# Optimization experiments

Hardware: AMD Instinct MI355X
Metric: run time of the kernel (lower is better)

The kernel has to match this reference:

```python
import jax, jax.numpy as jnp
import numpy as np
from math import sqrt

DIM = 64
N_HEADS = 12
B, T = 4, 2048


def setup_inputs() -> dict:
    key = jax.random.key(0)
    ks = jax.random.split(key, 5)
    scale = 1.0 / sqrt(DIM)
    x = jax.random.normal(ks[0], (B, T, DIM), dtype=jnp.float32)
    # torch Linear(dim, h*dim) weight is (h*dim, dim); store transposed (dim, h*dim)
    Wq = jax.random.uniform(ks[1], (DIM, N_HEADS * DIM), dtype=jnp.float32, minval=-scale, maxval=scale)
    Wk = jax.random.uniform(ks[2], (DIM, N_HEADS * DIM), dtype=jnp.float32, minval=-scale, maxval=scale)
    Wv = jax.random.uniform(ks[3], (DIM, N_HEADS * DIM), dtype=jnp.float32, minval=-scale, maxval=scale)
    # finalDense: Linear(h*dim, dim) -> stored (h*dim, dim)
    Wo = jax.random.uniform(ks[4], (N_HEADS * DIM, DIM), dtype=jnp.float32,
                            minval=-1.0 / sqrt(N_HEADS * DIM), maxval=1.0 / sqrt(N_HEADS * DIM))
    return {"x": x, "Wq": Wq, "Wk": Wk, "Wv": Wv, "Wo": Wo}


def reference(x, Wq, Wk, Wv, Wo):
    b, t, k = x.shape
    h = Wq.shape[1] // k
    # NOTE: the original module does .view(b,t,h,k).view(b*h,t,k), a flat
    # row-major memory reinterpretation (NOT a head transpose). jnp.reshape
    # is the same flat reshape, so this is faithful.
    Q = (x @ Wq).reshape(b * h, t, k)
    K = (x @ Wk).reshape(b * h, t, k)
    V = (x @ Wv).reshape(b * h, t, k)
    # W[b,i,j] = sum_k K[b,i,k] * Q[b,j,k], scaled; softmax over j (last dim)
    W = jnp.einsum('bik,bjk->bij', K, Q) / sqrt(k)
    W = jax.nn.softmax(W, axis=2)
    Z = jnp.einsum('bij,bjk->bik', W, V)  # (b*h, t, k)
    Z = Z.reshape(b, t, h * k)  # flat reinterpretation, matches torch views
    return Z @ Wo
```

## Files before the change

kernel.cpp:

```cpp
#include <hip/hip_runtime.h>
#include <hip/hip_bf16.h>


#define DIM 64
#define NH 12
#define HD 768
#define BT 8192
#define TSEQ 2048
#define NSLICE 48
#define SLICE (TSEQ*DIM)

#define LDQ 72
#define LDP 72

typedef unsigned short ushort;
typedef __attribute__((ext_vector_type(8))) short bf16x8;
typedef __attribute__((ext_vector_type(4))) float f32x4;

__device__ __forceinline__ float b2f(ushort u) {
    union { unsigned int i; float f; } v; v.i = ((unsigned int)u) << 16; return v.f;
}
__device__ __forceinline__ ushort f2b(float f) {
    union { float f; unsigned int i; } v; v.f = f;
    unsigned int x = v.i;
    return (ushort)((x + 0x7fffu + ((x >> 16) & 1u)) >> 16);
}

__global__ __launch_bounds__(256) void prep_x(
    const float* __restrict__ x, ushort* __restrict__ xb)
{
    int idx = (blockIdx.x * 256 + threadIdx.x) * 8;
    float4 a = *(const float4*)&x[idx];
    float4 b = *(const float4*)&x[idx + 4];
    ushort tmp[8] __attribute__((aligned(16)));
    tmp[0]=f2b(a.x); tmp[1]=f2b(a.y); tmp[2]=f2b(a.z); tmp[3]=f2b(a.w);
    tmp[4]=f2b(b.x); tmp[5]=f2b(b.y); tmp[6]=f2b(b.z); tmp[7]=f2b(b.w);
    *(float4*)&xb[idx] = *(const float4*)tmp;
}

__global__ __launch_bounds__(256) void prep_w(
    const float* __restrict__ Wq, const float* __restrict__ Wk,
    const float* __restrict__ Wv, const float* __restrict__ Wo,
    ushort* __restrict__ Wt, ushort* __restrict__ Wot)
{
    __shared__ float tile[64][65];
    int bx = blockIdx.x, z = blockIdx.y;
    const float* __restrict__ IN = (z == 0) ? Wq : (z == 1) ? Wk : (z == 2) ? Wv : Wo;
    int inStride  = (z < 3) ? HD : DIM;
    int outStride = (z < 3) ? DIM : HD;
    int rbase = (z < 3) ? 0 : bx * 64;
    int cbase = (z < 3) ? bx * 64 : 0;
    ushort* __restrict__ OUT = (z < 3) ? (Wt + (size_t)z * HD * DIM) : Wot;
    int t = threadIdx.x;
    int r = t >> 2, c0 = (t & 3) * 16;
    #pragma unroll
    for (int cc = 0; cc < 16; cc += 4) {
        float4 a = *(const float4*)&IN[(size_t)(rbase + r) * inStride + cbase + c0 + cc];
        tile[r][c0 + cc] = a.x; tile[r][c0 + cc + 1] = a.y;
        tile[r][c0 + cc + 2] = a.z; tile[r][c0 + cc + 3] = a.w;
    }
    __syncthreads();
    int cl = t >> 2, r0 = (t & 3) * 16;
    ushort tmp[16] __attribute__((aligned(16)));
    #pragma unroll
    for (int rr = 0; rr < 16; ++rr) tmp[rr] = f2b(tile[r0 + rr][cl]);
    *(float4*)&OUT[(size_t)(cbase + cl) * outStride + rbase + r0] = *(const float4*)tmp;
    *(float4*)&OUT[(size_t)(cbase + cl) * outStride + rbase + r0 + 8] = *(const float4*)&tmp[8];
}

__global__ __launch_bounds__(256) void qkv_kernel(
    const ushort* __restrict__ xb, const ushort* __restrict__ Wt,
    ushort* __restrict__ Q, ushort* __restrict__ K, ushort* __restrict__ V)
{
    int rowbase = blockIdx.x * 64;
    int ct = blockIdx.y;
    int which = ct / 12;
    int col0 = (ct % 12) * 64;
    const ushort* __restrict__ Wz = Wt + (size_t)which * HD * DIM;
    ushort* __restrict__ Y = (which == 0) ? Q : (which == 1) ? K : V;
    int t = threadIdx.x, w = t >> 6, lane = t & 63;
    int ln = lane & 15, q = lane >> 4;
    int m0 = rowbase + w * 16;

    bf16x8 af0 = *(const bf16x8*)&xb[(size_t)(m0 + ln) * DIM + q * 8];
    bf16x8 af1 = *(const bf16x8*)&xb[(size_t)(m0 + ln) * DIM + 32 + q * 8];
    #pragma unroll
    for (int nt = 0; nt < 4; ++nt) {
        int n = col0 + nt * 16 + ln;
        bf16x8 bf0 = *(const bf16x8*)&Wz[(size_t)n * DIM + q * 8];
        bf16x8 bf1 = *(const bf16x8*)&Wz[(size_t)n * DIM + 32 + q * 8];
        f32x4 acc = (f32x4){0.f, 0.f, 0.f, 0.f};
        acc = __builtin_amdgcn_mfma_f32_16x16x32_bf16(af0, bf0, acc, 0, 0, 0);
        acc = __builtin_amdgcn_mfma_f32_16x16x32_bf16(af1, bf1, acc, 0, 0, 0);
        #pragma unroll
        for (int r = 0; r < 4; ++r)
            Y[(size_t)(m0 + q * 4 + r) * HD + col0 + nt * 16 + ln] = f2b(acc[r]);
    }
}

__global__ __launch_bounds__(256) void vtrans_kernel(
    const ushort* __restrict__ V, ushort* __restrict__ Vt)
{
    __shared__ ushort tile[64 * LDQ];
    int tt = blockIdx.x, s = blockIdx.y;
    const ushort* __restrict__ Vp = V + (size_t)s * SLICE;
    ushort* __restrict__ Vo = Vt + (size_t)s * SLICE;
    int t = threadIdx.x;
    int r = t >> 3, c = (t & 7) * 8;
    *(float4*)&tile[r * LDQ + c] =
        *(const float4*)&Vp[(size_t)(tt * 64 + r) * DIM + c];
    *(float4*)&tile[(r + 32) * LDQ + c] =
        *(const float4*)&Vp[(size_t)(tt * 64 + r + 32) * DIM + c];
    __syncthreads();
    ushort tmp[8] __attribute__((aligned(16)));
    #pragma unroll
    for (int cc = 0; cc < 8; ++cc) tmp[cc] = tile[(c + cc) * LDQ + r];
    *(float4*)&Vo[(size_t)r * TSEQ + tt * 64 + c] = *(const float4*)tmp;
    #pragma unroll
    for (int cc = 0; cc < 8; ++cc) tmp[cc] = tile[(c + cc) * LDQ + r + 32];
    *(float4*)&Vo[(size_t)(r + 32) * TSEQ + tt * 64 + c] = *(const float4*)tmp;
}

__global__ __launch_bounds__(256) void attn_kernel(
    const ushort* __restrict__ Qs, const ushort* __restrict__ Ks,
    const ushort* __restrict__ Vts, ushort* __restrict__ Zs)
{
    const float SCALE2 = 0.18033688011112042f;
    __shared__ ushort Qt[64 * LDQ];
    __shared__ ushort Vtile[64 * LDQ];
    __shared__ ushort Pw[128 * LDP];
    int itile = blockIdx.x, s = blockIdx.y;
    const ushort* __restrict__ Qp = Qs + (size_t)s * SLICE;
    const ushort* __restrict__ Kp = Ks + (size_t)s * SLICE;
    const ushort* __restrict__ Vp = Vts + (size_t)s * SLICE;
    ushort* __restrict__ Zp = Zs + (size_t)s * SLICE;
    int t = threadIdx.x, w = t >> 6, lane = t & 63;
    int ln = lane & 15, q = lane >> 4;

    bf16x8 kf[2][2];
    #pragma unroll
    for (int ih = 0; ih < 2; ++ih) {
        int i0 = itile * 128 + w * 32 + ih * 16 + ln;
        kf[ih][0] = *(const bf16x8*)&Kp[(size_t)i0 * DIM + q * 8];
        kf[ih][1] = *(const bf16x8*)&Kp[(size_t)i0 * DIM + 32 + q * 8];
    }

    f32x4 Of[2][4];
    #pragma unroll
    for (int ih = 0; ih < 2; ++ih)
        #pragma unroll
        for (int dt = 0; dt < 4; ++dt) Of[ih][dt] = (f32x4){0.f, 0.f, 0.f, 0.f};
    float lsum[2] = {0.f, 0.f};
    ushort* Pme = &Pw[w * 32 * LDP];

    int sr = t >> 3, sc = (t & 7) * 8;
    for (int jt = 0; jt < TSEQ; jt += 64) {
        __syncthreads();
        *(float4*)&Qt[sr * LDQ + sc] =
            *(const float4*)&Qp[(size_t)(jt + sr) * DIM + sc];
        *(float4*)&Qt[(sr + 32) * LDQ + sc] =
            *(const float4*)&Qp[(size_t)(jt + sr + 32) * DIM + sc];
        *(float4*)&Vtile[sr * LDQ + sc] =
            *(const float4*)&Vp[(size_t)sr * TSEQ + jt + sc];
        *(float4*)&Vtile[(sr + 32) * LDQ + sc] =
            *(const float4*)&Vp[(size_t)(sr + 32) * TSEQ + jt + sc];
        __syncthreads();

        f32x4 Sf[2][4];
        #pragma unroll
        for (int mt = 0; mt < 4; ++mt) {
            bf16x8 a0 = *(const bf16x8*)&Qt[(mt * 16 + ln) * LDQ + q * 8];
            bf16x8 a1 = *(const bf16x8*)&Qt[(mt * 16 + ln) * LDQ + 32 + q * 8];
            #pragma unroll
            for (int ih = 0; ih < 2; ++ih) {
                f32x4 acc = (f32x4){0.f, 0.f, 0.f, 0.f};
                acc = __builtin_amdgcn_mfma_f32_16x16x32_bf16(a0, kf[ih][0], acc, 0, 0, 0);
                acc = __builtin_amdgcn_mfma_f32_16x16x32_bf16(a1, kf[ih][1], acc, 0, 0, 0);
                Sf[ih][mt] = acc;
            }
        }
        #pragma unroll
        for (int ih = 0; ih < 2; ++ih) {
            #pragma unroll
            for (int mt = 0; mt < 4; ++mt) {
                float p0 = __builtin_amdgcn_exp2f(Sf[ih][mt][0] * SCALE2);
                float p1 = __builtin_amdgcn_exp2f(Sf[ih][mt][1] * SCALE2);
                float p2 = __builtin_amdgcn_exp2f(Sf[ih][mt][2] * SCALE2);
                float p3 = __builtin_amdgcn_exp2f(Sf[ih][mt][3] * SCALE2);
                lsum[ih] += (p0 + p1) + (p2 + p3);
                ushort4 pk;
                pk.x = f2b(p0); pk.y = f2b(p1); pk.z = f2b(p2); pk.w = f2b(p3);
                *(ushort4*)&Pme[(ih * 16 + ln) * LDP + mt * 16 + q * 4] = pk;
            }
        }
        bf16x8 pa[2][2];
        #pragma unroll
        for (int ih = 0; ih < 2; ++ih) {
            pa[ih][0] = *(const bf16x8*)&Pme[(ih * 16 + ln) * LDP + q * 8];
            pa[ih][1] = *(const bf16x8*)&Pme[(ih * 16 + ln) * LDP + 32 + q * 8];
        }
        #pragma unroll
        for (int dt = 0; dt < 4; ++dt) {
            bf16x8 vb0 = *(const bf16x8*)&Vtile[(dt * 16 + ln) * LDQ + q * 8];
            bf16x8 vb1 = *(const bf16x8*)&Vtile[(dt * 16 + ln) * LDQ + 32 + q * 8];
            #pragma unroll
            for (int ih = 0; ih < 2; ++ih) {
                Of[ih][dt] = __builtin_amdgcn_mfma_f32_16x16x32_bf16(pa[ih][0], vb0, Of[ih][dt], 0, 0, 0);
                Of[ih][dt] = __builtin_amdgcn_mfma_f32_16x16x32_bf16(pa[ih][1], vb1, Of[ih][dt], 0, 0, 0);
            }
        }
    }
    float linv_r[2][4];
    #pragma unroll
    for (int ih = 0; ih < 2; ++ih) {
        float l = lsum[ih];
        l += __shfl_xor(l, 16);
        l += __shfl_xor(l, 32);
        float linv = 1.f / l;
        #pragma unroll
        for (int r = 0; r < 4; ++r) linv_r[ih][r] = __shfl(linv, q * 4 + r);
    }
    #pragma unroll
    for (int ih = 0; ih < 2; ++ih)
        #pragma unroll
        for (int dt = 0; dt < 4; ++dt)
            #pragma unroll
            for (int r = 0; r < 4; ++r)
                Pme[(ih * 16 + q * 4 + r) * LDP + dt * 16 + ln] =
                    f2b(Of[ih][dt][r] * linv_r[ih][r]);
    __syncthreads();
    int zr = t >> 1, zc = (t & 1) * 32;
    size_t zoff = (size_t)(itile * 128 + zr) * DIM + zc;
    #pragma unroll
    for (int c4 = 0; c4 < 4; ++c4)
        *(float4*)&Zp[zoff + c4 * 8] = *(const float4*)&Pw[zr * LDP + zc + c4 * 8];
}

__global__ __launch_bounds__(64) void out_kernel(
    const ushort* __restrict__ Z, const ushort* __restrict__ Wot,
    float* __restrict__ out)
{
    int m0 = blockIdx.x * 16;
    int lane = threadIdx.x;
    int ln = lane & 15, q = lane >> 4;
    f32x4 acc[4];
    #pragma unroll
    for (int nt = 0; nt < 4; ++nt) acc[nt] = (f32x4){0.f, 0.f, 0.f, 0.f};
    for (int kc = 0; kc < 24; ++kc) {
        bf16x8 af = *(const bf16x8*)&Z[(size_t)(m0 + ln) * HD + kc * 32 + q * 8];
        #pragma unroll
        for (int nt = 0; nt < 4; ++nt) {
            bf16x8 bf = *(const bf16x8*)&Wot[(size_t)(nt * 16 + ln) * HD + kc * 32 + q * 8];
            acc[nt] = __builtin_amdgcn_mfma_f32_16x16x32_bf16(af, bf, acc[nt], 0, 0, 0);
        }
    }
    #pragma unroll
    for (int nt = 0; nt < 4; ++nt)
        #pragma unroll
        for (int r = 0; r < 4; ++r)
            out[(size_t)(m0 + q * 4 + r) * DIM + nt * 16 + ln] = acc[nt][r];
}

extern "C" void kernel_launch(void* const* d_in, const int* in_sizes, int n_in,
                              void* d_out, int out_size, void* d_ws, size_t ws_size,
                              hipStream_t stream)
{
    const float* x  = (const float*)d_in[0];
    const float* Wq = (const float*)d_in[1];
    const float* Wk = (const float*)d_in[2];
    const float* Wv = (const float*)d_in[3];
    const float* Wo = (const float*)d_in[4];
    float* out = (float*)d_out;

    const size_t n = (size_t)BT * HD;
    ushort* Q   = (ushort*)d_ws;
    ushort* K   = Q + n;
    ushort* V   = K + n;
    ushort* Vt  = V + n;
    ushort* xb  = Vt;
    ushort* Wt  = Vt + (size_t)BT * DIM;
    ushort* Wot = Vt + n;
    ushort* Z   = V;

    prep_x<<<256, 256, 0, stream>>>(x, xb);
    prep_w<<<dim3(12, 4), 256, 0, stream>>>(Wq, Wk, Wv, Wo, Wt, Wot);
    qkv_kernel<<<dim3(128, 36), 256, 0, stream>>>(xb, Wt, Q, K, V);
    vtrans_kernel<<<dim3(32, 48), 256, 0, stream>>>(V, Vt);
    attn_kernel<<<dim3(16, 48), 256, 0, stream>>>(Q, K, Vt, Z);
    out_kernel<<<512, 64, 0, stream>>>(Z, Wot, out);
}
```

Baseline: 208.3 us.

## Restructure attention to single-wave blocks reading Q/V directly, fuse prep kernels

Attention becomes 64-thread blocks, each owning 32 K rows. Q and Vt fragments are loaded straight from global memory into registers, which removes the shared-memory staging and both barriers per tile. The block index is remapped so that 8 slices interleave, likely for L2 locality. Other changes: the x and weight prep kernels merge into one launch, the V transpose uses an XOR-swizzled shared tile with vector stores, and out_kernel doubles rows per block to reuse the Wo fragments. The softmax row sum now adds the truncated bf16 values actually used in P·V. The risk is that each wave re-reads Q and V from L2 with no sharing across waves.

Result: slower. 310.7 us (+49.2%).

```diff
diff --git a/kernel.cpp b/kernel.cpp
--- a/kernel.cpp
+++ b/kernel.cpp
@@ -10,8 +10,8 @@
 #define NSLICE 48
 #define SLICE (TSEQ*DIM)
 
-#define LDQ 72
 #define LDP 72
+#define LDT 72
 
 typedef unsigned short ushort;
 typedef __attribute__((ext_vector_type(8))) short bf16x8;
@@ -26,32 +26,32 @@
     return (ushort)((x + 0x7fffu + ((x >> 16) & 1u)) >> 16);
 }
 
-__global__ __launch_bounds__(256) void prep_x(
-    const float* __restrict__ x, ushort* __restrict__ xb)
-{
-    int idx = (blockIdx.x * 256 + threadIdx.x) * 8;
-    float4 a = *(const float4*)&x[idx];
-    float4 b = *(const float4*)&x[idx + 4];
-    ushort tmp[8] __attribute__((aligned(16)));
-    tmp[0]=f2b(a.x); tmp[1]=f2b(a.y); tmp[2]=f2b(a.z); tmp[3]=f2b(a.w);
-    tmp[4]=f2b(b.x); tmp[5]=f2b(b.y); tmp[6]=f2b(b.z); tmp[7]=f2b(b.w);
-    *(float4*)&xb[idx] = *(const float4*)tmp;
-}
-
-__global__ __launch_bounds__(256) void prep_w(
+__global__ __launch_bounds__(256) void prep_kernel(
+    const float* __restrict__ x,
     const float* __restrict__ Wq, const float* __restrict__ Wk,
     const float* __restrict__ Wv, const float* __restrict__ Wo,
-    ushort* __restrict__ Wt, ushort* __restrict__ Wot)
+    ushort* __restrict__ xb, ushort* __restrict__ Wt, ushort* __restrict__ Wot)
 {
     __shared__ float tile[64][65];
-    int bx = blockIdx.x, z = blockIdx.y;
+    int bx = blockIdx.x;
+    int t = threadIdx.x;
+    if (bx >= 48) {
+        int idx = ((bx - 48) * 256 + t) * 8;
+        float4 a = *(const float4*)&x[idx];
+        float4 b = *(const float4*)&x[idx + 4];
+        ushort tmp[8] __attribute__((aligned(16)));
+        tmp[0]=f2b(a.x); tmp[1]=f2b(a.y); tmp[2]=f2b(a.z); tmp[3]=f2b(a.w);
+        tmp[4]=f2b(b.x); tmp[5]=f2b(b.y); tmp[6]=f2b(b.z); tmp[7]=f2b(b.w);
+        *(float4*)&xb[idx] = *(const float4*)tmp;
+        return;
+    }
+    int z = bx / 12, bt = bx % 12;
     const float* __restrict__ IN = (z == 0) ? Wq : (z == 1) ? Wk : (z == 2) ? Wv : Wo;
     int inStride  = (z < 3) ? HD : DIM;
     int outStride = (z < 3) ? DIM : HD;
-    int rbase = (z < 3) ? 0 : bx * 64;
-    int cbase = (z < 3) ? bx * 64 : 0;
+    int rbase = (z < 3) ? 0 : bt * 64;
+    int cbase = (z < 3) ? bt * 64 : 0;
     ushort* __restrict__ OUT = (z < 3) ? (Wt + (size_t)z * HD * DIM) : Wot;
-    int t = threadIdx.x;
     int r = t >> 2, c0 = (t & 3) * 16;
     #pragma unroll
     for (int cc = 0; cc < 16; cc += 4) {
@@ -101,97 +101,105 @@
 __global__ __launch_bounds__(256) void vtrans_kernel(
     const ushort* __restrict__ V, ushort* __restrict__ Vt)
 {
-    __shared__ ushort tile[64 * LDQ];
+    __shared__ ushort tileT[64 * LDT];
     int tt = blockIdx.x, s = blockIdx.y;
     const ushort* __restrict__ Vp = V + (size_t)s * SLICE;
     ushort* __restrict__ Vo = Vt + (size_t)s * SLICE;
     int t = threadIdx.x;
     int r = t >> 3, c = (t & 7) * 8;
-    *(float4*)&tile[r * LDQ + c] =
-        *(const float4*)&Vp[(size_t)(tt * 64 + r) * DIM + c];
-    *(float4*)&tile[(r + 32) * LDQ + c] =
-        *(const float4*)&Vp[(size_t)(tt * 64 + r + 32) * DIM + c];
+    ushort va[8] __attribute__((aligned(16)));
+    ushort vb[8] __attribute__((aligned(16)));
+    *(float4*)va = *(const float4*)&Vp[(size_t)(tt * 64 + r) * DIM + c];
+    *(float4*)vb = *(const float4*)&Vp[(size_t)(tt * 64 + r + 32) * DIM + c];
+    int g0 = ((r >> 3) ^ (c >> 3)) * 8 + (r & 7);
+    int g1 = (((r + 32) >> 3) ^ (c >> 3)) * 8 + (r & 7);
+    #pragma unroll
+    for (int k = 0; k < 8; ++k) {
+        tileT[(c + k) * LDT + g0] = va[k];
+        tileT[(c + k) * LDT + g1] = vb[k];
+    }
     __syncthreads();
-    ushort tmp[8] __attribute__((aligned(16)));
-    #pragma unroll
-    for (int cc = 0; cc < 8; ++cc) tmp[cc] = tile[(c + cc) * LDQ + r];
-    *(float4*)&Vo[(size_t)r * TSEQ + tt * 64 + c] = *(const float4*)tmp;
-    #pragma unroll
-    for (int cc = 0; cc < 8; ++cc) tmp[cc] = tile[(c + cc) * LDQ + r + 32];
-    *(float4*)&Vo[(size_t)(r + 32) * TSEQ + tt * 64 + c] = *(const float4*)tmp;
-}
-
-__global__ __launch_bounds__(256) void attn_kernel(
+    #pragma unroll
+    for (int j = 0; j < 2; ++j) {
+        int flat = t + 256 * j;
+        int d = flat >> 3, tg = flat & 7;
+        int sg = tg ^ ((d >> 3) & 7);
+        float4 vv = *(const float4*)&tileT[d * LDT + sg * 8];
+        *(float4*)&Vo[(size_t)d * TSEQ + tt * 64 + tg * 8] = vv;
+    }
+}
+
+__global__ __launch_bounds__(64) void attn_kernel(
     const ushort* __restrict__ Qs, const ushort* __restrict__ Ks,
     const ushort* __restrict__ Vts, ushort* __restrict__ Zs)
 {
     const float SCALE2 = 0.18033688011112042f;
-    __shared__ ushort Qt[64 * LDQ];
-    __shared__ ushort Vtile[64 * LDQ];
-    __shared__ ushort Pw[128 * LDP];
-    int itile = blockIdx.x, s = blockIdx.y;
+    __shared__ ushort Pme[32 * LDP];
+    int bid = blockIdx.x;
+    int s = (bid >> 9) * 8 + (bid & 7);
+    int itile = (bid >> 3) & 63;
     const ushort* __restrict__ Qp = Qs + (size_t)s * SLICE;
     const ushort* __restrict__ Kp = Ks + (size_t)s * SLICE;
     const ushort* __restrict__ Vp = Vts + (size_t)s * SLICE;
     ushort* __restrict__ Zp = Zs + (size_t)s * SLICE;
-    int t = threadIdx.x, w = t >> 6, lane = t & 63;
+    int lane = threadIdx.x;
     int ln = lane & 15, q = lane >> 4;
 
     bf16x8 kf[2][2];
     #pragma unroll
     for (int ih = 0; ih < 2; ++ih) {
-        int i0 = itile * 128 + w * 32 + ih * 16 + ln;
+        int i0 = itile * 32 + ih * 16 + ln;
         kf[ih][0] = *(const bf16x8*)&Kp[(size_t)i0 * DIM + q * 8];
         kf[ih][1] = *(const bf16x8*)&Kp[(size_t)i0 * DIM + 32 + q * 8];
     }
-
     f32x4 Of[2][4];
     #pragma unroll
     for (int ih = 0; ih < 2; ++ih)
         #pragma unroll
         for (int dt = 0; dt < 4; ++dt) Of[ih][dt] = (f32x4){0.f, 0.f, 0.f, 0.f};
     float lsum[2] = {0.f, 0.f};
-    ushort* Pme = &Pw[w * 32 * LDP];
-
-    int sr = t >> 3, sc = (t & 7) * 8;
+
     for (int jt = 0; jt < TSEQ; jt += 64) {
-        __syncthreads();
-        *(float4*)&Qt[sr * LDQ + sc] =
-            *(const float4*)&Qp[(size_t)(jt + sr) * DIM + sc];
-        *(float4*)&Qt[(sr + 32) * LDQ + sc] =
-            *(const float4*)&Qp[(size_t)(jt + sr + 32) * DIM + sc];
-        *(float4*)&Vtile[sr * LDQ + sc] =
-            *(const float4*)&Vp[(size_t)sr * TSEQ + jt + sc];
-        *(float4*)&Vtile[(sr + 32) * LDQ + sc] =
-            *(const float4*)&Vp[(size_t)(sr + 32) * TSEQ + jt + sc];
-        __syncthreads();
-
-        f32x4 Sf[2][4];
+        bf16x8 aq[4][2];
         #pragma unroll
         for (int mt = 0; mt < 4; ++mt) {
-            bf16x8 a0 = *(const bf16x8*)&Qt[(mt * 16 + ln) * LDQ + q * 8];
-            bf16x8 a1 = *(const bf16x8*)&Qt[(mt * 16 + ln) * LDQ + 32 + q * 8];
-            #pragma unroll
-            for (int ih = 0; ih < 2; ++ih) {
+            aq[mt][0] = *(const bf16x8*)&Qp[(size_t)(jt + mt * 16 + ln) * DIM + q * 8];
+            aq[mt][1] = *(const bf16x8*)&Qp[(size_t)(jt + mt * 16 + ln) * DIM + 32 + q * 8];
+        }
+        bf16x8 vb[4][2];
+        #pragma unroll
+        for (int dt = 0; dt < 4; ++dt) {
+            vb[dt][0] = *(const bf16x8*)&Vp[(size_t)(dt * 16 + ln) * TSEQ + jt + q * 8];
+            vb[dt][1] = *(const bf16x8*)&Vp[(size_t)(dt * 16 + ln) * TSEQ + jt + 32 + q * 8];
+        }
+        #pragma unroll
+        for (int ih = 0; ih < 2; ++ih) {
+            f32x4 Sf[4];
+            #pragma unroll
+            for (int mt = 0; mt < 4; ++mt) {
                 f32x4 acc = (f32x4){0.f, 0.f, 0.f, 0.f};
-                acc = __builtin_amdgcn_mfma_f32_16x16x32_bf16(a0, kf[ih][0], acc, 0, 0, 0);
-                acc = __builtin_amdgcn_mfma_f32_16x16x32_bf16(a1, kf[ih][1], acc, 0, 0, 0);
-                Sf[ih][mt] = acc;
+                acc = __builtin_amdgcn_mfma_f32_16x16x32_bf16(aq[mt][0], kf[ih][0], acc, 0, 0, 0);
+                acc = __builtin_amdgcn_mfma_f32_16x16x32_bf16(aq[mt][1], kf[ih][1], acc, 0, 0, 0);
+                Sf[mt] = acc;
             }
-        }
-        #pragma unroll
-        for (int ih = 0; ih < 2; ++ih) {
+            float ls = 0.f;
             #pragma unroll
             for (int mt = 0; mt < 4; ++mt) {
-                float p0 = __builtin_amdgcn_exp2f(Sf[ih][mt][0] * SCALE2);
-                float p1 = __builtin_amdgcn_exp2f(Sf[ih][mt][1] * SCALE2);
-                float p2 = __builtin_amdgcn_exp2f(Sf[ih][mt][2] * SCALE2);
-                float p3 = __builtin_amdgcn_exp2f(Sf[ih][mt][3] * SCALE2);
-                lsum[ih] += (p0 + p1) + (p2 + p3);
-                ushort4 pk;
-                pk.x = f2b(p0); pk.y = f2b(p1); pk.z = f2b(p2); pk.w = f2b(p3);
-                *(ushort4*)&Pme[(ih * 16 + ln) * LDP + mt * 16 + q * 4] = pk;
+                float p0 = __builtin_amdgcn_exp2f(Sf[mt][0] * SCALE2);
+                float p1 = __builtin_amdgcn_exp2f(Sf[mt][1] * SCALE2);
+                float p2 = __builtin_amdgcn_exp2f(Sf[mt][2] * SCALE2);
+                float p3 = __builtin_amdgcn_exp2f(Sf[mt][3] * SCALE2);
+                unsigned int b0 = __float_as_uint(p0), b1 = __float_as_uint(p1);
+                unsigned int b2 = __float_as_uint(p2), b3 = __float_as_uint(p3);
+                unsigned int t1 = b1 & 0xFFFF0000u, t3 = b3 & 0xFFFF0000u;
+                unsigned int h01 = (b0 >> 16) | t1;
+                unsigned int h23 = (b2 >> 16) | t3;
+                ls += __uint_as_float(h01 << 16) + __uint_as_float(t1)
+                    + __uint_as_float(h23 << 16) + __uint_as_float(t3);
+                *(uint2*)&Pme[(ih * 16 + ln) * LDP + mt * 16 + q * 4] =
+                    make_uint2(h01, h23);
             }
+            lsum[ih] += ls;
         }
         bf16x8 pa[2][2];
         #pragma unroll
@@ -200,15 +208,12 @@
             pa[ih][1] = *(const bf16x8*)&Pme[(ih * 16 + ln) * LDP + 32 + q * 8];
         }
         #pragma unroll
-        for (int dt = 0; dt < 4; ++dt) {
-            bf16x8 vb0 = *(const bf16x8*)&Vtile[(dt * 16 + ln) * LDQ + q * 8];
-            bf16x8 vb1 = *(const bf16x8*)&Vtile[(dt * 16 + ln) * LDQ + 32 + q * 8];
+        for (int dt = 0; dt < 4; ++dt)
             #pragma unroll
             for (int ih = 0; ih < 2; ++ih) {
-                Of[ih][dt] = __builtin_amdgcn_mfma_f32_16x16x32_bf16(pa[ih][0], vb0, Of[ih][dt], 0, 0, 0);
-                Of[ih][dt] = __builtin_amdgcn_mfma_f32_16x16x32_bf16(pa[ih][1], vb1, Of[ih][dt], 0, 0, 0);
+                Of[ih][dt] = __builtin_amdgcn_mfma_f32_16x16x32_bf16(pa[ih][0], vb[dt][0], Of[ih][dt], 0, 0, 0);
+                Of[ih][dt] = __builtin_amdgcn_mfma_f32_16x16x32_bf16(pa[ih][1], vb[dt][1], Of[ih][dt], 0, 0, 0);
             }
-        }
     }
     float linv_r[2][4];
     #pragma unroll
@@ -228,37 +233,43 @@
             for (int r = 0; r < 4; ++r)
                 Pme[(ih * 16 + q * 4 + r) * LDP + dt * 16 + ln] =
                     f2b(Of[ih][dt][r] * linv_r[ih][r]);
-    __syncthreads();
-    int zr = t >> 1, zc = (t & 1) * 32;
-    size_t zoff = (size_t)(itile * 128 + zr) * DIM + zc;
+    int row = lane >> 1, half = lane & 1;
+    size_t zoff = (size_t)(itile * 32 + row) * DIM + half * 32;
     #pragma unroll
     for (int c4 = 0; c4 < 4; ++c4)
-        *(float4*)&Zp[zoff + c4 * 8] = *(const float4*)&Pw[zr * LDP + zc + c4 * 8];
+        *(float4*)&Zp[zoff + c4 * 8] =
+            *(const float4*)&Pme[row * LDP + half * 32 + c4 * 8];
 }
 
 __global__ __launch_bounds__(64) void out_kernel(
     const ushort* __restrict__ Z, const ushort* __restrict__ Wot,
     float* __restrict__ out)
 {
-    int m0 = blockIdx.x * 16;
+    int m0 = blockIdx.x * 32;
     int lane = threadIdx.x;
     int ln = lane & 15, q = lane >> 4;
-    f32x4 acc[4];
-    #pragma unroll
-    for (int nt = 0; nt < 4; ++nt) acc[nt] = (f32x4){0.f, 0.f, 0.f, 0.f};
+    f32x4 acc[2][4];
+    #pragma unroll
+    for (int u = 0; u < 2; ++u)
+        #pragma unroll
+        for (int nt = 0; nt < 4; ++nt) acc[u][nt] = (f32x4){0.f, 0.f, 0.f, 0.f};
     for (int kc = 0; kc < 24; ++kc) {
-        bf16x8 af = *(const bf16x8*)&Z[(size_t)(m0 + ln) * HD + kc * 32 + q * 8];
+        bf16x8 a0 = *(const bf16x8*)&Z[(size_t)(m0 + ln) * HD + kc * 32 + q * 8];
+        bf16x8 a1 = *(const bf16x8*)&Z[(size_t)(m0 + 16 + ln) * HD + kc * 32 + q * 8];
         #pragma unroll
         for (int nt = 0; nt < 4; ++nt) {
             bf16x8 bf = *(const bf16x8*)&Wot[(size_t)(nt * 16 + ln) * HD + kc * 32 + q * 8];
-            acc[nt] = __builtin_amdgcn_mfma_f32_16x16x32_bf16(af, bf, acc[nt], 0, 0, 0);
-        }
-    }
-    #pragma unroll
-    for (int nt = 0; nt < 4; ++nt)
-        #pragma unroll
-        for (int r = 0; r < 4; ++r)
-            out[(size_t)(m0 + q * 4 + r) * DIM + nt * 16 + ln] = acc[nt][r];
+            acc[0][nt] = __builtin_amdgcn_mfma_f32_16x16x32_bf16(a0, bf, acc[0][nt], 0, 0, 0);
+            acc[1][nt] = __builtin_amdgcn_mfma_f32_16x16x32_bf16(a1, bf, acc[1][nt], 0, 0, 0);
+        }
+    }
+    #pragma unroll
+    for (int u = 0; u < 2; ++u)
+        #pragma unroll
+        for (int nt = 0; nt < 4; ++nt)
+            #pragma unroll
+            for (int r = 0; r < 4; ++r)
+                out[(size_t)(m0 + u * 16 + q * 4 + r) * DIM + nt * 16 + ln] = acc[u][nt][r];
 }
 
 extern "C" void kernel_launch(void* const* d_in, const int* in_sizes, int n_in,
@@ -282,10 +293,9 @@
     ushort* Wot = Vt + n;
     ushort* Z   = V;
 
-    prep_x<<<256, 256, 0, stream>>>(x, xb);
-    prep_w<<<dim3(12, 4), 256, 0, stream>>>(Wq, Wk, Wv, Wo, Wt, Wot);
+    prep_kernel<<<304, 256, 0, stream>>>(x, Wq, Wk, Wv, Wo, xb, Wt, Wot);
     qkv_kernel<<<dim3(128, 36), 256, 0, stream>>>(xb, Wt, Q, K, V);
     vtrans_kernel<<<dim3(32, 48), 256, 0, stream>>>(V, Vt);
-    attn_kernel<<<dim3(16, 48), 256, 0, stream>>>(Q, K, Vt, Z);
-    out_kernel<<<512, 64, 0, stream>>>(Z, Wot, out);
-}
+    attn_kernel<<<3072, 64, 0, stream>>>(Q, K, Vt, Z);
+    out_kernel<<<256, 64, 0, stream>>>(Z, Wot, out);
+}
```
